# Kernel tuning notes

Measured on AMD Instinct MI355X. Metric: run time of the kernel, lower is better.

The kernel has to match this reference:

```python
import math
import jax, jax.numpy as jnp
import numpy as np

B, S, D, H = 2, 2048, 1024, 16
HD = D // H
I = 3752  # round(1024 * 11/3 / 8) * 8, per GluMLP default
EPS = 1e-6


def _alibi_bias(nheads, n):
    # AlibiPostionEmbedding: slopes (power-of-2 formula) * -1, times |i-j|
    start = 2.0 ** (-(2.0 ** (-(math.log2(nheads) - 3))))
    slopes = np.array([start * start ** i for i in range(nheads)], dtype=np.float64) * -1.0
    pos = np.arange(n)
    rel = np.abs(pos[None, :] - pos[:, None])  # [n, n]
    return jnp.asarray(slopes[:, None, None] * rel[None, :, :], dtype=jnp.float32)


def rmsnorm(h, w):
    h32 = h.astype(jnp.float32)
    var = jnp.mean(h32 * h32, axis=-1, keepdims=True)
    return (w * (h32 * jax.lax.rsqrt(var + EPS))).astype(h.dtype)


def setup_inputs() -> dict:
    key = jax.random.key(0)
    ks = jax.random.split(key, 16)
    sd = 1.0 / math.sqrt(D)
    si = 1.0 / math.sqrt(I)
    rn = lambda k, shape, s: jax.random.normal(k, shape, jnp.float32) * s
    return {
        "x": rn(ks[0], (B, S, D), 1.0),
        "wq": rn(ks[1], (D, D), sd), "bq": rn(ks[2], (D,), 0.02),
        "wk": rn(ks[3], (D, D), sd), "bk": rn(ks[4], (D,), 0.02),
        "wv": rn(ks[5], (D, D), sd), "bv": rn(ks[6], (D,), 0.02),
        "wo": rn(ks[7], (D, D), sd), "bo": rn(ks[8], (D,), 0.02),
        "w_gate": rn(ks[9], (D, I), sd),
        "w_up": rn(ks[10], (D, I), sd),
        "w_down": rn(ks[11], (I, D), si),
        "ln1_w": jnp.ones((D,), jnp.float32),
        "ln2_w": jnp.ones((D,), jnp.float32),
        "attn_bias": _alibi_bias(H, S),                       # [H, S, S]
        "tgt_mask": jnp.triu(jnp.ones((S, S), bool), 1),      # causal, True = masked
        "key_padding_mask": jnp.zeros((B, S), bool),          # True = padded
    }


def reference(x, wq, bq, wk, bk, wv, bv, wo, bo, w_gate, w_up, w_down,
              ln1_w, ln2_w, attn_bias, tgt_mask, key_padding_mask):
    # ---- TransformerEncoderLayer.forward (eval mode: dropout = identity) ----
    residual = x
    h = rmsnorm(x, ln1_w)
    # MultiheadAttention with ALiBi bias + fused bool masks
    q = (h @ wq + bq).reshape(B, S, H, HD)
    k = (h @ wk + bk).reshape(B, S, H, HD)
    v = (h @ wv + bv).reshape(B, S, H, HD)
    scores = jnp.einsum("bqhd,bkhd->bhqk", q, k) * (HD ** -0.5)  # [B,H,S,S]
    scores = scores + attn_bias[None]
    mask = tgt_mask[None, :, :] | key_padding_mask[:, None, :]   # [B,S,S]
    scores = jnp.where(mask[:, None, :, :], -jnp.inf, scores)
    probs = jax.nn.softmax(scores, axis=-1)
    attn = jnp.einsum("bhqk,bkhd->bqhd", probs, v).reshape(B, S, D)
    attn = attn @ wo + bo
    residual = attn + residual
    # GluMLP (SwiGLU)
    h2 = rmsnorm(residual, ln2_w)
    mlp = (jax.nn.silu(h2 @ w_gate) * (h2 @ w_up)) @ w_down
    return mlp + residual
```

## Files before the change

kernel.cpp:

```cpp
#include <hip/hip_runtime.h>
#include <hip/hip_bf16.h>
#include <cmath>

typedef __bf16 bf16_t;
typedef __bf16 bf16x8 __attribute__((ext_vector_type(8)));
typedef short  s16x8  __attribute__((ext_vector_type(8)));
typedef float  f32x4  __attribute__((ext_vector_type(4)));

static constexpr int Bn  = 2;
static constexpr int Sn  = 2048;
static constexpr int Dn  = 1024;
static constexpr int Hn  = 16;
static constexpr int In  = 3752;
static constexpr int Mn  = Bn * Sn;
static constexpr int Ipad = 3840;

__device__ __forceinline__ void cp16(const bf16_t* g, bf16_t* l) {
  __builtin_amdgcn_global_load_lds(
      (const __attribute__((address_space(1))) unsigned int*)g,
      (__attribute__((address_space(3))) unsigned int*)l, 16, 0, 0);
}

__device__ __forceinline__ void xcd_map(int bid, int nM, int nN, int& m, int& n) {
  const int q = (nM * nN) >> 3;
  const int L = (bid & 7) * q + (bid >> 3);
  const int bandw = nN << 3;
  const int band = L / bandw;
  const int rem  = L - band * bandw;
  n = rem >> 3;
  m = (band << 3) + (rem & 7);
}

struct TransJob  { const float* src; bf16_t* dst; int R, C, bx, start; };
struct TransJobs { TransJob j[7]; };

__global__ __launch_bounds__(256) void k_transpose_all(TransJobs jobs) {
  const int bid = blockIdx.x;
  int jj = 0;
#pragma unroll
  for (int t = 1; t < 7; ++t)
    if (bid >= jobs.j[t].start) jj = t;
  const TransJob jb = jobs.j[jj];
  const int local = bid - jb.start;
  const int r0 = (local / jb.bx) * 32, c0 = (local % jb.bx) * 32;
  __shared__ float tile[32][33];
  const int tx = threadIdx.x & 31, ty = threadIdx.x >> 5;
#pragma unroll
  for (int e = 0; e < 4; ++e) {
    int r = r0 + ty + e * 8, c = c0 + tx;
    if (r < jb.R && c < jb.C) tile[ty + e * 8][tx] = jb.src[(size_t)r * jb.C + c];
  }
  __syncthreads();
#pragma unroll
  for (int e = 0; e < 4; ++e) {
    int c = c0 + ty + e * 8, r = r0 + tx;
    if (r < jb.R && c < jb.C) jb.dst[(size_t)c * jb.R + r] = (bf16_t)tile[tx][ty + e * 8];
  }
}

__global__ __launch_bounds__(256) void k_rmsnorm(const float* __restrict__ in,
                                                 const float* __restrict__ w,
                                                 bf16_t* __restrict__ out) {
  const int row = blockIdx.x;
  const int tid = threadIdx.x;
  const float* ip = in + (size_t)row * Dn;
  float v[4];
  float ss = 0.f;
#pragma unroll
  for (int e = 0; e < 4; ++e) {
    v[e] = ip[tid + e * 256];
    ss += v[e] * v[e];
  }
  for (int off = 32; off > 0; off >>= 1) ss += __shfl_down(ss, off);
  __shared__ float red[4];
  if ((tid & 63) == 0) red[tid >> 6] = ss;
  __syncthreads();
  float tot = red[0] + red[1] + red[2] + red[3];
  float sc = rsqrtf(tot * (1.0f / Dn) + 1e-6f);
  bf16_t* op = out + (size_t)row * Dn;
#pragma unroll
  for (int e = 0; e < 4; ++e) {
    int idx = tid + e * 256;
    op[idx] = (bf16_t)(w[idx] * v[e] * sc);
  }
}

template <int MODE>
__global__ __launch_bounds__(512, 2) void k_gemm256(
    const bf16_t* __restrict__ A, const bf16_t* __restrict__ Bt,
    const float* __restrict__ b0, const float* __restrict__ b1,
    const float* __restrict__ b2, const bf16_t* __restrict__ gsrc,
    bf16_t* __restrict__ out, int ldo, int Nb) {
  __shared__ bf16_t As[3][256 * 32];
  __shared__ bf16_t Bs[3][256 * 32];
  const int m0 = blockIdx.x * 256, n0 = blockIdx.y * 256;
  const int tid = threadIdx.x;
  const int lane = tid & 63, w = tid >> 6;
  const int wm = w >> 2, wn = w & 3;
  const int l15 = lane & 15, quad = lane >> 4;
  const int sw2 = (l15 >> 1) & 3;
  const int slr = lane >> 2, slc = lane & 3;

  int arow[2], brow[2], chk[2], slab[2];
#pragma unroll
  for (int c = 0; c < 2; ++c) {
    const int r = (w * 2 + c) * 16 + slr;
    arow[c] = m0 + r;
    brow[c] = min(n0 + r, Nb - 1);
    chk[c]  = (slc ^ ((r >> 1) & 3)) * 8;
    slab[c] = (w * 2 + c) * 512;
  }

  f32x4 acc[8][4];
  const f32x4 z4 = {0.f, 0.f, 0.f, 0.f};
#pragma unroll
  for (int i = 0; i < 8; ++i)
#pragma unroll
    for (int j = 0; j < 4; ++j) acc[i][j] = z4;

  constexpr int NT = Dn / 32;

  auto stage = [&](int t) {
    const int bi = t - (t / 3) * 3;
    const int k0 = t * 32;
#pragma unroll
    for (int c = 0; c < 2; ++c) {
      cp16(A  + (size_t)arow[c] * Dn + k0 + chk[c], &As[bi][slab[c]]);
      cp16(Bt + (size_t)brow[c] * Dn + k0 + chk[c], &Bs[bi][slab[c]]);
    }
  };

  stage(0);
  stage(1);
  asm volatile("s_waitcnt vmcnt(4)" ::: "memory");
  asm volatile("s_barrier" ::: "memory");

  for (int t = 0; t < NT; ++t) {
    const int bi = t - (t / 3) * 3;
    if (t + 2 < NT) stage(t + 2);

    bf16x8 af[8], bfr[4];
#pragma unroll
    for (int j = 0; j < 4; ++j) {
      const int r2 = wn * 64 + j * 16 + l15;
      bfr[j] = *(const bf16x8*)(&Bs[bi][r2 * 32 + ((quad ^ sw2) * 8)]);
    }
#pragma unroll
    for (int i = 0; i < 8; ++i) {
      const int r2 = wm * 128 + i * 16 + l15;
      af[i] = *(const bf16x8*)(&As[bi][r2 * 32 + ((quad ^ sw2) * 8)]);
    }
    __builtin_amdgcn_s_setprio(1);
#pragma unroll
    for (int i = 0; i < 8; ++i)
#pragma unroll
      for (int j = 0; j < 4; ++j)
        acc[i][j] = __builtin_amdgcn_mfma_f32_16x16x32_bf16(af[i], bfr[j], acc[i][j], 0, 0, 0);
    __builtin_amdgcn_s_setprio(0);

    if (t + 2 < NT) asm volatile("s_waitcnt vmcnt(4)" ::: "memory");
    else            asm volatile("s_waitcnt vmcnt(0)" ::: "memory");
    asm volatile("s_barrier" ::: "memory");
  }

#pragma unroll
  for (int i = 0; i < 8; ++i)
#pragma unroll
    for (int j = 0; j < 4; ++j) {
      const int col = n0 + wn * 64 + j * 16 + l15;
      float bval = 0.f;
      if (MODE == 0) {
        const int sel = col >> 10;
        bval = (sel == 0) ? b0[col] : (sel == 1) ? b1[col - 1024] : b2[col - 2048];
      }
#pragma unroll
      for (int r = 0; r < 4; ++r) {
        const int row = m0 + wm * 128 + i * 16 + quad * 4 + r;
        if (MODE == 0) {
          out[(size_t)row * ldo + col] = (bf16_t)(acc[i][j][r] + bval);
        } else if (MODE == 1) {
          out[(size_t)row * ldo + col] = (bf16_t)acc[i][j][r];
        } else {
          const float g = (float)gsrc[(size_t)row * ldo + col];
          const float sl = g / (1.f + expf(-g));
          const float val = sl * acc[i][j][r];
          out[(size_t)row * ldo + col] = (col < In) ? (bf16_t)val : (bf16_t)0.f;
        }
      }
    }
}

__global__ __launch_bounds__(256) void k_gemm64(
    const bf16_t* __restrict__ A, const bf16_t* __restrict__ Bt,
    const float* __restrict__ bias, const float* __restrict__ resid,
    float* __restrict__ outf, int N, int K, int lda, int ldb, int nN) {
  __shared__ bf16_t As[64 * 64];
  __shared__ bf16_t Bs[128 * 64];
  int mblk, nblk;
  xcd_map(blockIdx.x, Mn / 64, nN, mblk, nblk);
  const int m0 = mblk * 64, n0 = nblk * 128;
  const int tid = threadIdx.x;
  const int lane = tid & 63, wid = tid >> 6;
  const int wc = wid * 32;
  const int l15 = lane & 15, quad = lane >> 4;
  const int sw = l15 & 7;
  const int srow_lo = lane >> 3, pchunk = lane & 7;

  f32x4 acc[4][2];
  const f32x4 z4 = {0.f, 0.f, 0.f, 0.f};
#pragma unroll
  for (int i = 0; i < 4; ++i)
#pragma unroll
    for (int j = 0; j < 2; ++j) acc[i][j] = z4;

  for (int k0 = 0; k0 < K; k0 += 64) {
#pragma unroll
    for (int c = 0; c < 2; ++c) {
      const int r = (wid * 2 + c) * 8 + srow_lo;
      const int gc = pchunk ^ (r & 7);
      cp16(A + (size_t)(m0 + r) * lda + k0 + gc * 8, As + (wid * 2 + c) * 512);
    }
#pragma unroll
    for (int c = 0; c < 4; ++c) {
      const int r = (wid * 4 + c) * 8 + srow_lo;
      const int gc = pchunk ^ (r & 7);
      cp16(Bt + (size_t)(n0 + r) * ldb + k0 + gc * 8, Bs + (wid * 4 + c) * 512);
    }
    __syncthreads();
#pragma unroll
    for (int kh = 0; kh < 2; ++kh) {
      const int ph = ((kh * 4 + quad) ^ sw) * 8;
      bf16x8 af[4], bfr[2];
#pragma unroll
      for (int i = 0; i < 4; ++i)
        af[i] = *(const bf16x8*)(As + (i * 16 + l15) * 64 + ph);
#pragma unroll
      for (int j = 0; j < 2; ++j)
        bfr[j] = *(const bf16x8*)(Bs + (wc + j * 16 + l15) * 64 + ph);
#pragma unroll
      for (int i = 0; i < 4; ++i)
#pragma unroll
        for (int j = 0; j < 2; ++j)
          acc[i][j] = __builtin_amdgcn_mfma_f32_16x16x32_bf16(af[i], bfr[j], acc[i][j], 0, 0, 0);
    }
    __syncthreads();
  }

#pragma unroll
  for (int i = 0; i < 4; ++i)
#pragma unroll
    for (int j = 0; j < 2; ++j) {
      const int col = n0 + wc + j * 16 + l15;
      const float bval = bias ? bias[col] : 0.f;
#pragma unroll
      for (int r = 0; r < 4; ++r) {
        const int row = m0 + i * 16 + quad * 4 + r;
        const size_t idx = (size_t)row * N + col;
        outf[idx] = acc[i][j][r] + bval + (resid ? resid[idx] : 0.f);
      }
    }
}

__global__ __launch_bounds__(256) void k_attn(
    const bf16_t* __restrict__ qkv, bf16_t* __restrict__ Ob) {
  const int qt = (int)gridDim.x - 1 - (int)blockIdx.x;
  const int h  = blockIdx.y;
  const int b  = blockIdx.z;
  constexpr int LDK = 72, LDP = 76;
  __shared__ bf16_t Ks[64 * LDK];
  __shared__ bf16_t Vt[64 * LDK];
  __shared__ bf16_t Ps[4][32 * LDP];

  const int tid  = threadIdx.x;
  const int lane = tid & 63, w = tid >> 6;
  const int l15  = lane & 15, quad = lane >> 4;

  constexpr float L2E = 1.4426950408889634f;
  const float slopeL = -exp2f(-0.5f * (float)(h + 1)) * L2E;

  bf16x8 aq[2][2];
#pragma unroll
  for (int g = 0; g < 2; ++g) {
    const int row = qt * 128 + w * 32 + g * 16 + l15;
    const bf16_t* qp = qkv + (size_t)(b * Sn + row) * 3072 + h * 64;
    aq[g][0] = *(const bf16x8*)(qp + quad * 8);
    aq[g][1] = *(const bf16x8*)(qp + 32 + quad * 8);
#pragma unroll
    for (int e = 0; e < 8; ++e) {
      aq[g][0][e] = (bf16_t)((float)aq[g][0][e] * 0.125f);
      aq[g][1][e] = (bf16_t)((float)aq[g][1][e] * 0.125f);
    }
  }

  int qrow[2];
  float rowterm[2][4];
#pragma unroll
  for (int g = 0; g < 2; ++g) {
    qrow[g] = qt * 128 + w * 32 + g * 16 + quad * 4;
#pragma unroll
    for (int rr = 0; rr < 4; ++rr) rowterm[g][rr] = slopeL * (float)(qrow[g] + rr);
  }
  float colbase[4];
#pragma unroll
  for (int t = 0; t < 4; ++t) colbase[t] = slopeL * (float)(t * 16 + l15);

  f32x4 o[2][4], lacc[2];
  const f32x4 z4 = {0.f, 0.f, 0.f, 0.f};
#pragma unroll
  for (int g = 0; g < 2; ++g) {
    lacc[g] = z4;
#pragma unroll
    for (int dt = 0; dt < 4; ++dt) o[g][dt] = z4;
  }
  bf16x8 ones;
#pragma unroll
  for (int e = 0; e < 8; ++e) ones[e] = (bf16_t)1.0f;

  const int r = tid >> 2, c0e = (tid & 3) * 16;
  const size_t kbase = (size_t)(b * Sn + r) * 3072 + 1024 + h * 64 + c0e;
  const size_t step  = (size_t)64 * 3072;

  s16x8 kr0 = *(const s16x8*)(qkv + kbase);
  s16x8 kr1 = *(const s16x8*)(qkv + kbase + 8);
  s16x8 vr0 = *(const s16x8*)(qkv + kbase + 1024);
  s16x8 vr1 = *(const s16x8*)(qkv + kbase + 1024 + 8);

  const int nkt = 2 * qt + 2;
  for (int kt = 0; kt < nkt; ++kt) {
    __syncthreads();
    *(s16x8*)(Ks + r * LDK + c0e)     = kr0;
    *(s16x8*)(Ks + r * LDK + c0e + 8) = kr1;
    {
      const bf16x8 v0 = *(const bf16x8*)&vr0, v1 = *(const bf16x8*)&vr1;
#pragma unroll
      for (int e = 0; e < 8; ++e) {
        Vt[(c0e + e) * LDK + r]     = v0[e];
        Vt[(c0e + 8 + e) * LDK + r] = v1[e];
      }
    }
    __syncthreads();
    if (kt + 1 < nkt) {
      const size_t kb = kbase + (size_t)(kt + 1) * step;
      kr0 = *(const s16x8*)(qkv + kb);
      kr1 = *(const s16x8*)(qkv + kb + 8);
      vr0 = *(const s16x8*)(qkv + kb + 1024);
      vr1 = *(const s16x8*)(qkv + kb + 1024 + 8);
    }

    const float kofs = slopeL * (float)(kt * 64);
    const bool diag = (kt + 2 >= nkt);

#pragma unroll
    for (int g = 0; g < 2; ++g) {
      f32x4 s[4];
#pragma unroll
      for (int t = 0; t < 4; ++t) s[t] = z4;
#pragma unroll
      for (int t = 0; t < 4; ++t) {
        bf16x8 bk0 = *(const bf16x8*)(Ks + (t * 16 + l15) * LDK + quad * 8);
        bf16x8 bk1 = *(const bf16x8*)(Ks + (t * 16 + l15) * LDK + 32 + quad * 8);
        s[t] = __builtin_amdgcn_mfma_f32_16x16x32_bf16(aq[g][0], bk0, s[t], 0, 0, 0);
        s[t] = __builtin_amdgcn_mfma_f32_16x16x32_bf16(aq[g][1], bk1, s[t], 0, 0, 0);
      }
#pragma unroll
      for (int t = 0; t < 4; ++t) {
        const int j = kt * 64 + t * 16 + l15;
#pragma unroll
        for (int rr = 0; rr < 4; ++rr) {
          float v2 = fmaf(s[t][rr], L2E, rowterm[g][rr] - (kofs + colbase[t]));
          if (diag && j > qrow[g] + rr) v2 = -3.0e38f;
          Ps[w][(g * 16 + quad * 4 + rr) * LDP + t * 16 + l15] = (bf16_t)exp2f(v2);
        }
      }
    }

#pragma unroll
    for (int g = 0; g < 2; ++g) {
#pragma unroll
      for (int kh = 0; kh < 2; ++kh) {
        bf16x8 pa = *(const bf16x8*)(Ps[w] + (g * 16 + l15) * LDP + kh * 32 + quad * 8);
        lacc[g] = __builtin_amdgcn_mfma_f32_16x16x32_bf16(pa, ones, lacc[g], 0, 0, 0);
#pragma unroll
        for (int dt = 0; dt < 4; ++dt) {
          bf16x8 bv = *(const bf16x8*)(Vt + (dt * 16 + l15) * LDK + kh * 32 + quad * 8);
          o[g][dt] = __builtin_amdgcn_mfma_f32_16x16x32_bf16(pa, bv, o[g][dt], 0, 0, 0);
        }
      }
    }
  }

#pragma unroll
  for (int g = 0; g < 2; ++g)
#pragma unroll
    for (int rr = 0; rr < 4; ++rr) {
      const float inv = 1.f / lacc[g][rr];
      bf16_t* op = Ob + (size_t)(b * Sn + qrow[g] + rr) * 1024 + h * 64;
#pragma unroll
      for (int dt = 0; dt < 4; ++dt)
        op[dt * 16 + l15] = (bf16_t)(o[g][dt][rr] * inv);
    }
}

extern "C" void kernel_launch(void* const* d_in, const int* in_sizes, int n_in,
                              void* d_out, int out_size, void* d_ws, size_t ws_size,
                              hipStream_t stream) {
  (void)in_sizes; (void)n_in; (void)out_size; (void)ws_size;
  const float* x   = (const float*)d_in[0];
  const float* wq  = (const float*)d_in[1];
  const float* bq  = (const float*)d_in[2];
  const float* wk_ = (const float*)d_in[3];
  const float* bk  = (const float*)d_in[4];
  const float* wv  = (const float*)d_in[5];
  const float* bv  = (const float*)d_in[6];
  const float* wo  = (const float*)d_in[7];
  const float* bo  = (const float*)d_in[8];
  const float* wg  = (const float*)d_in[9];
  const float* wu  = (const float*)d_in[10];
  const float* wd  = (const float*)d_in[11];
  const float* ln1 = (const float*)d_in[12];
  const float* ln2 = (const float*)d_in[13];

  char* base = (char*)d_ws;
  const size_t MiB = 1024 * 1024;
  bf16_t* h1    = (bf16_t*)(base);
  bf16_t* wqkvT = (bf16_t*)(base + 8   * MiB);
  bf16_t* woT   = (bf16_t*)(base + 16  * MiB);
  bf16_t* wgT   = (bf16_t*)(base + 24  * MiB);
  bf16_t* wuT   = (bf16_t*)(base + 32  * MiB);
  bf16_t* wdT   = (bf16_t*)(base + 40  * MiB);
  bf16_t* qkvb  = (bf16_t*)(base + 48  * MiB);
  float*  res1  = (float*) (base + 72  * MiB);
  bf16_t* mlp   = (bf16_t*)(base + 88  * MiB);
  bf16_t* gbuf  = (bf16_t*)(base + 120 * MiB);
  bf16_t* attnb = (bf16_t*)d_out;
  bf16_t* h2    = (bf16_t*)d_out;

  const dim3 blk(256);
  const dim3 blk512(512);

  TransJobs jobs;
  int start = 0;
  auto setjob = [&](int idx, const float* s, bf16_t* d, int R, int C) {
    const int bx = (C + 31) / 32, by = (R + 31) / 32;
    jobs.j[idx] = {s, d, R, C, bx, start};
    start += bx * by;
  };
  setjob(0, wq,  wqkvT,                       Dn, Dn);
  setjob(1, wk_, wqkvT + (size_t)Dn * Dn,     Dn, Dn);
  setjob(2, wv,  wqkvT + 2 * (size_t)Dn * Dn, Dn, Dn);
  setjob(3, wo,  woT, Dn, Dn);
  setjob(4, wg,  wgT, Dn, In);
  setjob(5, wu,  wuT, Dn, In);
  setjob(6, wd,  wdT, In, Dn);
  k_transpose_all<<<dim3(start), blk, 0, stream>>>(jobs);

  k_rmsnorm<<<dim3(Mn), blk, 0, stream>>>(x, ln1, h1);

  k_gemm256<0><<<dim3(Mn / 256, 3072 / 256), blk512, 0, stream>>>(
      h1, wqkvT, bq, bk, bv, nullptr, qkvb, 3072, 3072);

  k_attn<<<dim3(Sn / 128, Hn, Bn), blk, 0, stream>>>(qkvb, attnb);

  k_gemm64<<<dim3((Mn / 64) * (Dn / 128)), blk, 0, stream>>>(
      attnb, woT, bo, x, res1, Dn, Dn, Dn, Dn, Dn / 128);

  k_rmsnorm<<<dim3(Mn), blk, 0, stream>>>(res1, ln2, h2);

  k_gemm256<1><<<dim3(Mn / 256, Ipad / 256), blk512, 0, stream>>>(
      h2, wgT, nullptr, nullptr, nullptr, nullptr, gbuf, Ipad, In);

  k_gemm256<2><<<dim3(Mn / 256, Ipad / 256), blk512, 0, stream>>>(
      h2, wuT, nullptr, nullptr, nullptr, gbuf, mlp, Ipad, In);

  k_gemm64<<<dim3((Mn / 64) * (Dn / 128)), blk, 0, stream>>>(
      mlp, wdT, nullptr, res1, (float*)d_out, Dn, Ipad, Ipad, In, Dn / 128);
}
```

Before: 714.3 us.

## Fuse gate and up projections into one dual-accumulator GEMM kernel

Replaces the two separate gate and up GEMM launches, which wrote the gate result to a bf16 buffer and then re-read it, with one kernel. It loads each A tile once and multiplies it against both the gate and up weight tiles, keeping two accumulator sets and applying SiLU(g)*u in the epilogue. This removes a full intermediate write and read plus a second pass over the A operand. The cost is a smaller 128x128 tile with 256 threads and double the accumulator registers, which may hurt occupancy and MFMA efficiency compared with the 256x256 tile kernel.

```diff
diff --git a/kernel.cpp b/kernel.cpp
--- a/kernel.cpp
+++ b/kernel.cpp
@@ -89,7 +89,7 @@
 __global__ __launch_bounds__(512, 2) void k_gemm256(
     const bf16_t* __restrict__ A, const bf16_t* __restrict__ Bt,
     const float* __restrict__ b0, const float* __restrict__ b1,
-    const float* __restrict__ b2, const bf16_t* __restrict__ gsrc,
+    const float* __restrict__ b2,
     bf16_t* __restrict__ out, int ldo, int Nb) {
   __shared__ bf16_t As[3][256 * 32];
   __shared__ bf16_t Bs[3][256 * 32];
@@ -176,16 +176,102 @@
 #pragma unroll
       for (int r = 0; r < 4; ++r) {
         const int row = m0 + wm * 128 + i * 16 + quad * 4 + r;
-        if (MODE == 0) {
-          out[(size_t)row * ldo + col] = (bf16_t)(acc[i][j][r] + bval);
-        } else if (MODE == 1) {
-          out[(size_t)row * ldo + col] = (bf16_t)acc[i][j][r];
-        } else {
-          const float g = (float)gsrc[(size_t)row * ldo + col];
-          const float sl = g / (1.f + expf(-g));
-          const float val = sl * acc[i][j][r];
-          out[(size_t)row * ldo + col] = (col < In) ? (bf16_t)val : (bf16_t)0.f;
-        }
+        out[(size_t)row * ldo + col] = (bf16_t)(acc[i][j][r] + bval);
+      }
+    }
+}
+
+__global__ __launch_bounds__(256, 2) void k_gateup(
+    const bf16_t* __restrict__ A, const bf16_t* __restrict__ Bg,
+    const bf16_t* __restrict__ Bu, bf16_t* __restrict__ out) {
+  __shared__ bf16_t As[3][128 * 32];
+  __shared__ bf16_t Gs[3][128 * 32];
+  __shared__ bf16_t Us[3][128 * 32];
+  const int m0 = blockIdx.x * 128, n0 = blockIdx.y * 128;
+  const int tid = threadIdx.x;
+  const int lane = tid & 63, w = tid >> 6;
+  const int wm = w >> 1, wn = w & 1;
+  const int l15 = lane & 15, quad = lane >> 4;
+  const int sw2 = (l15 >> 1) & 3;
+
+  int arow[2], brow[2], chk[2], slab[2];
+#pragma unroll
+  for (int c = 0; c < 2; ++c) {
+    const int r = (tid >> 2) + 64 * c;
+    arow[c] = m0 + r;
+    brow[c] = min(n0 + r, In - 1);
+    chk[c]  = ((tid & 3) ^ ((r >> 1) & 3)) * 8;
+    slab[c] = c * 2048 + w * 512;
+  }
+
+  f32x4 accg[4][4], accu[4][4];
+  const f32x4 z4 = {0.f, 0.f, 0.f, 0.f};
+#pragma unroll
+  for (int i = 0; i < 4; ++i)
+#pragma unroll
+    for (int j = 0; j < 4; ++j) { accg[i][j] = z4; accu[i][j] = z4; }
+
+  constexpr int NT = Dn / 32;
+
+  auto stage = [&](int t) {
+    const int bi = t - (t / 3) * 3;
+    const int k0 = t * 32;
+#pragma unroll
+    for (int c = 0; c < 2; ++c) {
+      cp16(A  + (size_t)arow[c] * Dn + k0 + chk[c], &As[bi][slab[c]]);
+      cp16(Bg + (size_t)brow[c] * Dn + k0 + chk[c], &Gs[bi][slab[c]]);
+      cp16(Bu + (size_t)brow[c] * Dn + k0 + chk[c], &Us[bi][slab[c]]);
+    }
+  };
+
+  stage(0);
+  stage(1);
+  asm volatile("s_waitcnt vmcnt(6)" ::: "memory");
+  asm volatile("s_barrier" ::: "memory");
+
+  for (int t = 0; t < NT; ++t) {
+    const int bi = t - (t / 3) * 3;
+    if (t + 2 < NT) stage(t + 2);
+
+    bf16x8 af[4], gf[4], uf[4];
+#pragma unroll
+    for (int i = 0; i < 4; ++i) {
+      const int r2 = wm * 64 + i * 16 + l15;
+      af[i] = *(const bf16x8*)(&As[bi][r2 * 32 + ((quad ^ sw2) * 8)]);
+    }
+#pragma unroll
+    for (int j = 0; j < 4; ++j) {
+      const int r2 = wn * 64 + j * 16 + l15;
+      gf[j] = *(const bf16x8*)(&Gs[bi][r2 * 32 + ((quad ^ sw2) * 8)]);
+      uf[j] = *(const bf16x8*)(&Us[bi][r2 * 32 + ((quad ^ sw2) * 8)]);
+    }
+    __builtin_amdgcn_s_setprio(1);
+#pragma unroll
+    for (int i = 0; i < 4; ++i)
+#pragma unroll
+      for (int j = 0; j < 4; ++j) {
+        accg[i][j] = __builtin_amdgcn_mfma_f32_16x16x32_bf16(af[i], gf[j], accg[i][j], 0, 0, 0);
+        accu[i][j] = __builtin_amdgcn_mfma_f32_16x16x32_bf16(af[i], uf[j], accu[i][j], 0, 0, 0);
+      }
+    __builtin_amdgcn_s_setprio(0);
+
+    if (t + 2 < NT) asm volatile("s_waitcnt vmcnt(6)" ::: "memory");
+    else            asm volatile("s_waitcnt vmcnt(0)" ::: "memory");
+    asm volatile("s_barrier" ::: "memory");
+  }
+
+#pragma unroll
+  for (int i = 0; i < 4; ++i)
+#pragma unroll
+    for (int j = 0; j < 4; ++j) {
+      const int col = n0 + wn * 64 + j * 16 + l15;
+#pragma unroll
+      for (int r = 0; r < 4; ++r) {
+        const int row = m0 + wm * 64 + i * 16 + quad * 4 + r;
+        const float g = accg[i][j][r];
+        const float u = accu[i][j][r];
+        const float sl = g / (1.f + expf(-g));
+        out[(size_t)row * Ipad + col] = (col < In) ? (bf16_t)(sl * u) : (bf16_t)0.f;
       }
     }
 }
@@ -431,7 +517,6 @@
   bf16_t* qkvb  = (bf16_t*)(base + 48  * MiB);
   float*  res1  = (float*) (base + 72  * MiB);
   bf16_t* mlp   = (bf16_t*)(base + 88  * MiB);
-  bf16_t* gbuf  = (bf16_t*)(base + 120 * MiB);
   bf16_t* attnb = (bf16_t*)d_out;
   bf16_t* h2    = (bf16_t*)d_out;
 
@@ -457,7 +542,7 @@
   k_rmsnorm<<<dim3(Mn), blk, 0, stream>>>(x, ln1, h1);
 
   k_gemm256<0><<<dim3(Mn / 256, 3072 / 256), blk512, 0, stream>>>(
-      h1, wqkvT, bq, bk, bv, nullptr, qkvb, 3072, 3072);
+      h1, wqkvT, bq, bk, bv, qkvb, 3072, 3072);
 
   k_attn<<<dim3(Sn / 128, Hn, Bn), blk, 0, stream>>>(qkvb, attnb);
 
@@ -466,11 +551,7 @@
 
   k_rmsnorm<<<dim3(Mn), blk, 0, stream>>>(res1, ln2, h2);
 
-  k_gemm256<1><<<dim3(Mn / 256, Ipad / 256), blk512, 0, stream>>>(
-      h2, wgT, nullptr, nullptr, nullptr, nullptr, gbuf, Ipad, In);
-
-  k_gemm256<2><<<dim3(Mn / 256, Ipad / 256), blk512, 0, stream>>>(
-      h2, wuT, nullptr, nullptr, nullptr, gbuf, mlp, Ipad, In);
+  k_gateup<<<dim3(Mn / 128, Ipad / 128), blk, 0, stream>>>(h2, wgT, wuT, mlp);
 
   k_gemm64<<<dim3((Mn / 64) * (Dn / 128)), blk, 0, stream>>>(
       mlp, wdT, nullptr, res1, (float*)d_out, Dn, Ipad, Ipad, In, Dn / 128);
```

Result: faster. 693.1 us (-3.0%).
